# Kernel optimization log

Measured on AMD Instinct MI355X. Metric: run time of the kernel, lower is better.

## Reference

```python
import jax, jax.numpy as jnp
import numpy as np

D_MODEL, D_HID, N_EXPERTS, TOP_K = 1024, 4096, 8, 2

def setup_inputs() -> dict:
    key = jax.random.key(0)
    ks = jax.random.split(key, 6)
    B, T = 2, 2048
    x = jax.random.normal(ks[0], (B, T, D_MODEL), dtype=jnp.float32)
    gate_w = jax.random.normal(ks[1], (N_EXPERTS, D_MODEL), dtype=jnp.float32) * (1.0 / np.sqrt(D_MODEL))
    # kaiming_uniform-ish init for expert weights
    lim1 = np.sqrt(6.0 / D_MODEL)
    lim2 = np.sqrt(6.0 / D_HID)
    w1 = jax.random.uniform(ks[2], (N_EXPERTS, D_MODEL, D_HID), dtype=jnp.float32, minval=-lim1, maxval=lim1)
    w2 = jax.random.uniform(ks[3], (N_EXPERTS, D_HID, D_MODEL), dtype=jnp.float32, minval=-lim2, maxval=lim2)
    b1 = jnp.zeros((N_EXPERTS, 1, D_HID), dtype=jnp.float32)
    b2 = jnp.zeros((N_EXPERTS, 1, D_MODEL), dtype=jnp.float32)
    return {"x": x, "gate_w": gate_w, "w1": w1, "b1": b1, "w2": w2, "b2": b2}

def reference(x, gate_w, w1, b1, w2, b2):
    B, T, D = x.shape
    E = gate_w.shape[0]
    xf = x.reshape(-1, D)                              # [N, D]
    N = xf.shape[0]
    # Router: logits -> softmax -> top-k -> renormalize
    logits = jnp.einsum('nd,ed->ne', xf, gate_w)       # [N, E]
    scores = jax.nn.softmax(logits, axis=-1)
    top_w, top_i = jax.lax.top_k(scores, TOP_K)        # [N, K]
    top_w = top_w / jnp.sum(top_w, axis=-1, keepdims=True)
    # Dense combine weights (zero for unselected experts) — same math as
    # the padded-bmm dispatch/combine: padded slots have weight 0.
    gates = jnp.zeros((N, E), xf.dtype).at[jnp.arange(N)[:, None], top_i].add(top_w)  # [N, E]
    # Grouped expert MLP (computed densely; weighted combine zeroes unrouted experts)
    h = jax.nn.gelu(jnp.einsum('nd,edh->enh', xf, w1) + b1, approximate=False)  # [E, N, H]
    expert_out = jnp.einsum('enh,ehd->end', h, w2) + b2                          # [E, N, D]
    out = jnp.einsum('end,ne->nd', expert_out, gates)                            # [N, D]
    return out.reshape(B, T, D)
```

## Files before the change

### kernel.cpp

```cpp
#include <hip/hip_runtime.h>
#include <math.h>

#define NTOK 4096
#define DM   1024
#define DH   4096
#define NE   8
#define NSLOT (NTOK*2)

typedef unsigned short u16;
typedef __attribute__((ext_vector_type(8))) short shortx8;
typedef __attribute__((ext_vector_type(4))) float floatx4;
typedef __attribute__((ext_vector_type(4))) int   intx4;

__device__ __forceinline__ u16 f2bf(float f) {
  union { float f; unsigned u; } c; c.f = f;
  unsigned r = c.u + 0x7fffu + ((c.u >> 16) & 1u);
  return (u16)(r >> 16);
}

__device__ __forceinline__ void async_cp16(const u16* g, u16* l) {
  __builtin_amdgcn_global_load_lds(
      (const __attribute__((address_space(1))) void*)g,
      (__attribute__((address_space(3))) void*)l, 16, 0, 0);
}

__global__ void cvt_x_kernel(const float* __restrict__ x, u16* __restrict__ xb) {
  int i = (blockIdx.x * 256 + threadIdx.x) * 8;
  float4 v0 = *(const float4*)(x + i);
  float4 v1 = *(const float4*)(x + i + 4);
  u16 tmp[8] = {f2bf(v0.x), f2bf(v0.y), f2bf(v0.z), f2bf(v0.w),
                f2bf(v1.x), f2bf(v1.y), f2bf(v1.z), f2bf(v1.w)};
  *(intx4*)(xb + i) = *(intx4*)tmp;
}

template<int K, int NW>
__global__ void transpose_kernel(const float* __restrict__ W, u16* __restrict__ Wt) {
  int e = blockIdx.z;
  const float* Wp = W + (size_t)e * K * NW;
  u16* Wtp = Wt + (size_t)e * K * NW;
  int n = blockIdx.x * 64 + (threadIdx.x & 63);
  int kend = blockIdx.y * 256 + 256;
  for (int k0 = blockIdx.y * 256 + (threadIdx.x >> 6) * 8; k0 < kend; k0 += 32) {
    u16 tmp[8];
#pragma unroll
    for (int j = 0; j < 8; j++) tmp[j] = f2bf(Wp[(size_t)(k0 + j) * NW + n]);
    *(intx4*)(Wtp + (size_t)n * K + k0) = *(intx4*)tmp;
  }
}

__global__ __launch_bounds__(256) void router_kernel(const float* __restrict__ x,
                                                     const float* __restrict__ gw,
                                                     int* __restrict__ eos,
                                                     float* __restrict__ wos) {
  int wave = threadIdx.x >> 6, lane = threadIdx.x & 63;
  int n = blockIdx.x * 4 + wave;
  const float* xr = x + (size_t)n * DM;
  float acc[NE];
#pragma unroll
  for (int e = 0; e < NE; e++) acc[e] = 0.f;
  for (int d = lane; d < DM; d += 64) {
    float xv = xr[d];
#pragma unroll
    for (int e = 0; e < NE; e++) acc[e] += xv * gw[e * DM + d];
  }
#pragma unroll
  for (int e = 0; e < NE; e++) {
    float v = acc[e];
#pragma unroll
    for (int off = 32; off > 0; off >>= 1) v += __shfl_xor(v, off, 64);
    acc[e] = v;
  }
  if (lane == 0) {
    int i0 = 0;
    for (int e = 1; e < NE; e++) if (acc[e] > acc[i0]) i0 = e;
    int i1 = (i0 == 0) ? 1 : 0;
    for (int e = 0; e < NE; e++) { if (e == i0) continue; if (acc[e] > acc[i1]) i1 = e; }
    float e1 = expf(acc[i1] - acc[i0]);
    float w0 = 1.f / (1.f + e1);
    eos[2 * n] = i0;  eos[2 * n + 1] = i1;
    wos[2 * n] = w0;  wos[2 * n + 1] = 1.f - w0;
  }
}

__global__ __launch_bounds__(256) void build_groups_kernel(
    const int* __restrict__ eos, const float* __restrict__ wos,
    int* __restrict__ goff, int* __restrict__ tok_of_g, float* __restrict__ w_of_g) {
  __shared__ int pref[256][NE];
  __shared__ int tot[NE];
  __shared__ int ebase[NE + 1];
  int t = threadIdx.x;
  int c[NE];
#pragma unroll
  for (int e = 0; e < NE; e++) c[e] = 0;
  for (int i = 0; i < NSLOT / 256; i++) {
    int e = eos[t * (NSLOT / 256) + i];
#pragma unroll
    for (int q = 0; q < NE; q++) if (e == q) c[q]++;
  }
#pragma unroll
  for (int e = 0; e < NE; e++) pref[t][e] = c[e];
  __syncthreads();
  if (t < NE) {
    int run = 0;
    for (int i = 0; i < 256; i++) { int v = pref[i][t]; pref[i][t] = run; run += v; }
    tot[t] = run;
  }
  __syncthreads();
  if (t == 0) {
    int o = 0;
    for (int e = 0; e < NE; e++) { ebase[e] = o; o += tot[e]; }
    ebase[NE] = o;
  }
  __syncthreads();
  int off[NE];
#pragma unroll
  for (int e = 0; e < NE; e++) off[e] = ebase[e] + pref[t][e];
  for (int i = 0; i < NSLOT / 256; i++) {
    int s = t * (NSLOT / 256) + i;
    int e = eos[s];
    int g = 0;
#pragma unroll
    for (int q = 0; q < NE; q++) if (e == q) { g = off[q]; off[q] = g + 1; }
    tok_of_g[g] = s >> 1;
    w_of_g[g] = wos[s];
  }
  if (t <= NE) goff[t] = ebase[t];
}

template<int K, int NOUT, int MODE>
__global__ __launch_bounds__(256) void moe_gemm(
    const u16* __restrict__ A, const u16* __restrict__ Wt, const float* __restrict__ bias,
    const int* __restrict__ goff, const int* __restrict__ tok_of_g,
    const float* __restrict__ w_of_g,
    u16* __restrict__ Hout, float* __restrict__ Out) {
  int e = blockIdx.z;
  int gb = goff[e];
  int cntE = goff[e + 1] - gb;
  int m0 = blockIdx.y * 128;
  if (m0 >= cntE) return;
  int mvalid = cntE - m0; if (mvalid > 128) mvalid = 128;
  int gbase = gb + m0;
  int n0 = blockIdx.x * 128;
  int tid = threadIdx.x;
  int lane = tid & 63, wave = tid >> 6;

  __shared__ __align__(16) u16 As[128 * 32];
  __shared__ __align__(16) u16 Bs[128 * 32];

  int sr = lane >> 2;
  int sc = (lane & 3) * 8;
  int ra0 = wave * 16 + sr;
  int ra1 = 64 + wave * 16 + sr;
  int ca0 = (ra0 < mvalid) ? ra0 : (mvalid - 1);
  int ca1 = (ra1 < mvalid) ? ra1 : (mvalid - 1);
  const u16 *pa0, *pa1;
  if (MODE == 0) {
    pa0 = A + (size_t)tok_of_g[gbase + ca0] * K + sc;
    pa1 = A + (size_t)tok_of_g[gbase + ca1] * K + sc;
  } else {
    pa0 = A + (size_t)(gbase + ca0) * K + sc;
    pa1 = A + (size_t)(gbase + ca1) * K + sc;
  }
  const u16* wte = Wt + (size_t)e * NOUT * K;
  const u16* pb0 = wte + (size_t)(n0 + ra0) * K + sc;
  const u16* pb1 = wte + (size_t)(n0 + ra1) * K + sc;
  u16* ldsA0 = As + wave * 512;
  u16* ldsA1 = As + 2048 + wave * 512;
  u16* ldsB0 = Bs + wave * 512;
  u16* ldsB1 = Bs + 2048 + wave * 512;

  int wm = wave >> 1, wn = wave & 1;
  int lr = lane & 15, lk = (lane >> 4) * 8;

  floatx4 acc[4][4];
#pragma unroll
  for (int i = 0; i < 4; i++)
#pragma unroll
    for (int j = 0; j < 4; j++) acc[i][j] = (floatx4){0.f, 0.f, 0.f, 0.f};

  for (int k0 = 0; k0 < K; k0 += 32) {
    __syncthreads();
    async_cp16(pa0 + k0, ldsA0);
    async_cp16(pa1 + k0, ldsA1);
    async_cp16(pb0 + k0, ldsB0);
    async_cp16(pb1 + k0, ldsB1);
    __syncthreads();
    shortx8 af[4], bfr[4];
#pragma unroll
    for (int i = 0; i < 4; i++) {
      af[i]  = *(const shortx8*)&As[(wm * 64 + i * 16 + lr) * 32 + lk];
      bfr[i] = *(const shortx8*)&Bs[(wn * 64 + i * 16 + lr) * 32 + lk];
    }
#pragma unroll
    for (int i = 0; i < 4; i++)
#pragma unroll
      for (int j = 0; j < 4; j++)
        acc[i][j] = __builtin_amdgcn_mfma_f32_16x16x32_bf16(af[i], bfr[j], acc[i][j], 0, 0, 0);
  }

  const float* bp = bias + (size_t)e * NOUT + n0;
  if (MODE == 0) {
#pragma unroll
    for (int i = 0; i < 4; i++) {
      int rowb = wm * 64 + i * 16 + (lane >> 4) * 4;
#pragma unroll
      for (int r = 0; r < 4; r++) {
        int grow = rowb + r;
        if (grow < mvalid) {
          size_t base = (size_t)(gbase + grow) * NOUT + n0;
#pragma unroll
          for (int j = 0; j < 4; j++) {
            int col = wn * 64 + j * 16 + lr;
            float v = acc[i][j][r] + bp[col];
            v = 0.5f * v * (1.f + erff(v * 0.70710678118654752f));
            Hout[base + col] = f2bf(v);
          }
        }
      }
    }
  } else {
#pragma unroll
    for (int i = 0; i < 4; i++) {
      int rowb = wm * 64 + i * 16 + (lane >> 4) * 4;
#pragma unroll
      for (int r = 0; r < 4; r++) {
        int grow = rowb + r;
        if (grow < mvalid) {
          int gi = gbase + grow;
          int t = tok_of_g[gi];
          float wg = w_of_g[gi];
          float* orow = Out + (size_t)t * DM + n0;
#pragma unroll
          for (int j = 0; j < 4; j++) {
            int col = wn * 64 + j * 16 + lr;
            atomicAdd(&orow[col], wg * (acc[i][j][r] + bp[col]));
          }
        }
      }
    }
  }
}

extern "C" void kernel_launch(void* const* d_in, const int* in_sizes, int n_in,
                              void* d_out, int out_size, void* d_ws, size_t ws_size,
                              hipStream_t stream) {
  const float* x  = (const float*)d_in[0];
  const float* gw = (const float*)d_in[1];
  const float* w1 = (const float*)d_in[2];
  const float* b1 = (const float*)d_in[3];
  const float* w2 = (const float*)d_in[4];
  const float* b2 = (const float*)d_in[5];
  float* out = (float*)d_out;
  char* ws = (char*)d_ws;

  u16* xb = (u16*)(ws + 0);
  u16* wt = (u16*)(ws + 8388608);
  u16* h  = (u16*)(ws + 75497472);
  char* meta = ws + 142606336;
  int*   eos      = (int*)(meta);
  int*   tok_of_g = (int*)(meta + 32768);
  float* wos      = (float*)(meta + 65536);
  float* w_of_g   = (float*)(meta + 98304);
  int*   goff     = (int*)(meta + 131072);

  hipMemsetAsync(out, 0, (size_t)NTOK * DM * 4, stream);

  cvt_x_kernel<<<NTOK * DM / 8 / 256, 256, 0, stream>>>(x, xb);
  transpose_kernel<DM, DH><<<dim3(DH / 64, DM / 256, NE), 256, 0, stream>>>(w1, wt);
  router_kernel<<<NTOK / 4, 256, 0, stream>>>(x, gw, eos, wos);
  build_groups_kernel<<<1, 256, 0, stream>>>(eos, wos, goff, tok_of_g, w_of_g);
  moe_gemm<DM, DH, 0><<<dim3(DH / 128, NTOK / 128, NE), 256, 0, stream>>>(
      xb, wt, b1, goff, tok_of_g, w_of_g, h, nullptr);
  transpose_kernel<DH, DM><<<dim3(DM / 64, DH / 256, NE), 256, 0, stream>>>(w2, wt);
  moe_gemm<DH, DM, 1><<<dim3(DM / 128, NTOK / 128, NE), 256, 0, stream>>>(
      h, wt, b2, goff, tok_of_g, w_of_g, nullptr, out);
}
```

Measured before the change: 693.4 us.

## Compact MoE GEMM tile list, split-K second GEMM, LDS-tiled weight transpose

The weight transpose now goes through an LDS tile, so global reads are coalesced float4 loads and writes are 16-byte chunks, instead of strided scalar reads. The router grouping builds a compact list of (expert, m-block) tiles, so the GEMMs launch only non-empty tiles rather than a sparse 3D grid full of early exits. The second GEMM splits K in two and accumulates both halves with atomics to raise occupancy. The trade-off is more atomic traffic on the output, and the fixed TMAX grid bound, which holds only when the number of tiles stays at or below 72.

```diff
diff --git a/kernel.cpp b/kernel.cpp
--- a/kernel.cpp
+++ b/kernel.cpp
@@ -6,6 +6,7 @@
 #define DH   4096
 #define NE   8
 #define NSLOT (NTOK*2)
+#define TMAX 72
 
 typedef unsigned short u16;
 typedef __attribute__((ext_vector_type(8))) short shortx8;
@@ -34,17 +35,34 @@
 }
 
 template<int K, int NW>
-__global__ void transpose_kernel(const float* __restrict__ W, u16* __restrict__ Wt) {
+__global__ __launch_bounds__(256) void transpose_kernel(const float* __restrict__ W,
+                                                        u16* __restrict__ Wt) {
+  __shared__ u16 tile[64][66];
   int e = blockIdx.z;
-  const float* Wp = W + (size_t)e * K * NW;
-  u16* Wtp = Wt + (size_t)e * K * NW;
-  int n = blockIdx.x * 64 + (threadIdx.x & 63);
-  int kend = blockIdx.y * 256 + 256;
-  for (int k0 = blockIdx.y * 256 + (threadIdx.x >> 6) * 8; k0 < kend; k0 += 32) {
-    u16 tmp[8];
-#pragma unroll
-    for (int j = 0; j < 8; j++) tmp[j] = f2bf(Wp[(size_t)(k0 + j) * NW + n]);
-    *(intx4*)(Wtp + (size_t)n * K + k0) = *(intx4*)tmp;
+  int n0 = blockIdx.x * 64, k0 = blockIdx.y * 64;
+  int tt = threadIdx.x;
+  const float* src = W + (size_t)e * K * NW + (size_t)(k0 + (tt >> 2)) * NW + n0 + (tt & 3) * 16;
+  int r = tt >> 2, c4 = (tt & 3) * 16;
+  float4 v[4];
+#pragma unroll
+  for (int i = 0; i < 4; i++) v[i] = *(const float4*)(src + i * 4);
+#pragma unroll
+  for (int i = 0; i < 4; i++) {
+    tile[r][c4 + 4 * i + 0] = f2bf(v[i].x);
+    tile[r][c4 + 4 * i + 1] = f2bf(v[i].y);
+    tile[r][c4 + 4 * i + 2] = f2bf(v[i].z);
+    tile[r][c4 + 4 * i + 3] = f2bf(v[i].w);
+  }
+  __syncthreads();
+  u16* dst = Wt + (size_t)e * NW * K + (size_t)n0 * K + k0;
+#pragma unroll
+  for (int p = 0; p < 2; p++) {
+    int n = (tt >> 3) + p * 32;
+    int kc = (tt & 7) * 8;
+    u16 o[8];
+#pragma unroll
+    for (int i = 0; i < 8; i++) o[i] = tile[kc + i][n];
+    *(intx4*)(dst + (size_t)n * K + kc) = *(intx4*)o;
   }
 }
 
@@ -84,7 +102,8 @@
 
 __global__ __launch_bounds__(256) void build_groups_kernel(
     const int* __restrict__ eos, const float* __restrict__ wos,
-    int* __restrict__ goff, int* __restrict__ tok_of_g, float* __restrict__ w_of_g) {
+    int* __restrict__ goff, int* __restrict__ tok_of_g, float* __restrict__ w_of_g,
+    int* __restrict__ tiles, int* __restrict__ ntiles) {
   __shared__ int pref[256][NE];
   __shared__ int tot[NE];
   __shared__ int ebase[NE + 1];
@@ -110,6 +129,10 @@
     int o = 0;
     for (int e = 0; e < NE; e++) { ebase[e] = o; o += tot[e]; }
     ebase[NE] = o;
+    int nt = 0;
+    for (int e = 0; e < NE; e++)
+      for (int mb = 0; mb * 128 < tot[e]; mb++) tiles[nt++] = (e << 16) | mb;
+    ntiles[0] = nt;
   }
   __syncthreads();
   int off[NE];
@@ -127,20 +150,27 @@
   if (t <= NE) goff[t] = ebase[t];
 }
 
-template<int K, int NOUT, int MODE>
+template<int K, int NOUT, int MODE, int KSPLIT>
 __global__ __launch_bounds__(256) void moe_gemm(
     const u16* __restrict__ A, const u16* __restrict__ Wt, const float* __restrict__ bias,
     const int* __restrict__ goff, const int* __restrict__ tok_of_g,
-    const float* __restrict__ w_of_g,
+    const float* __restrict__ w_of_g, const int* __restrict__ tiles,
+    const int* __restrict__ ntiles,
     u16* __restrict__ Hout, float* __restrict__ Out) {
-  int e = blockIdx.z;
+  const int KLEN = K / KSPLIT;
+  int tl = blockIdx.x;
+  if (tl >= ntiles[0]) return;
+  int packed = tiles[tl];
+  int e = packed >> 16;
+  int mb = packed & 0xffff;
+  int kseg = (KSPLIT > 1) ? blockIdx.z : 0;
   int gb = goff[e];
   int cntE = goff[e + 1] - gb;
-  int m0 = blockIdx.y * 128;
-  if (m0 >= cntE) return;
+  int m0 = mb * 128;
   int mvalid = cntE - m0; if (mvalid > 128) mvalid = 128;
   int gbase = gb + m0;
-  int n0 = blockIdx.x * 128;
+  int n0 = blockIdx.y * 128;
+  int kbeg = kseg * KLEN;
   int tid = threadIdx.x;
   int lane = tid & 63, wave = tid >> 6;
 
@@ -178,7 +208,7 @@
 #pragma unroll
     for (int j = 0; j < 4; j++) acc[i][j] = (floatx4){0.f, 0.f, 0.f, 0.f};
 
-  for (int k0 = 0; k0 < K; k0 += 32) {
+  for (int k0 = kbeg; k0 < kbeg + KLEN; k0 += 32) {
     __syncthreads();
     async_cp16(pa0 + k0, ldsA0);
     async_cp16(pa1 + k0, ldsA1);
@@ -233,7 +263,8 @@
 #pragma unroll
           for (int j = 0; j < 4; j++) {
             int col = wn * 64 + j * 16 + lr;
-            atomicAdd(&orow[col], wg * (acc[i][j][r] + bp[col]));
+            float bb = (kseg == 0) ? bp[col] : 0.f;
+            atomicAdd(&orow[col], wg * (acc[i][j][r] + bb));
           }
         }
       }
@@ -262,16 +293,18 @@
   float* wos      = (float*)(meta + 65536);
   float* w_of_g   = (float*)(meta + 98304);
   int*   goff     = (int*)(meta + 131072);
+  int*   tiles    = (int*)(meta + 131200);
+  int*   ntiles   = (int*)(meta + 131584);
 
   hipMemsetAsync(out, 0, (size_t)NTOK * DM * 4, stream);
 
   cvt_x_kernel<<<NTOK * DM / 8 / 256, 256, 0, stream>>>(x, xb);
-  transpose_kernel<DM, DH><<<dim3(DH / 64, DM / 256, NE), 256, 0, stream>>>(w1, wt);
+  transpose_kernel<DM, DH><<<dim3(DH / 64, DM / 64, NE), 256, 0, stream>>>(w1, wt);
   router_kernel<<<NTOK / 4, 256, 0, stream>>>(x, gw, eos, wos);
-  build_groups_kernel<<<1, 256, 0, stream>>>(eos, wos, goff, tok_of_g, w_of_g);
-  moe_gemm<DM, DH, 0><<<dim3(DH / 128, NTOK / 128, NE), 256, 0, stream>>>(
-      xb, wt, b1, goff, tok_of_g, w_of_g, h, nullptr);
-  transpose_kernel<DH, DM><<<dim3(DM / 64, DH / 256, NE), 256, 0, stream>>>(w2, wt);
-  moe_gemm<DH, DM, 1><<<dim3(DM / 128, NTOK / 128, NE), 256, 0, stream>>>(
-      h, wt, b2, goff, tok_of_g, w_of_g, nullptr, out);
-}
+  build_groups_kernel<<<1, 256, 0, stream>>>(eos, wos, goff, tok_of_g, w_of_g, tiles, ntiles);
+  moe_gemm<DM, DH, 0, 1><<<dim3(TMAX, DH / 128, 1), 256, 0, stream>>>(
+      xb, wt, b1, goff, tok_of_g, w_of_g, tiles, ntiles, h, nullptr);
+  transpose_kernel<DH, DM><<<dim3(DM / 64, DH / 64, NE), 256, 0, stream>>>(w2, wt);
+  moe_gemm<DH, DM, 1, 2><<<dim3(TMAX, DM / 128, 2), 256, 0, stream>>>(
+      h, wt, b2, goff, tok_of_g, w_of_g, tiles, ntiles, nullptr, out);
+}
```

New measurement: 685.0 us. No clear change (-1.2%).
